# Kernel optimization log

Measured on AMD Instinct MI355X. Metric: run time of the kernel, lower is better.

The kernel has to match this reference:

```python
import jax, jax.numpy as jnp
import numpy as np

MODES = 32
INPUT_MODES = 24
LAMBDA = 0.1
T_TOTAL = 1.0
EVAL_PTS = 200  # hardcoded in Circuit.forward


def _unitary_from_parameters(n, params):
    # Reconstruct a unitary from n**2-1 real SU(N)-generator coefficients:
    # Hermitian traceless H, then U = expm(iH) via eigh (differentiable).
    m = n * (n - 1) // 2
    re = params[:m]
    im = params[m:2 * m]
    d = params[2 * m:2 * m + n - 1]
    iu = jnp.triu_indices(n, 1)
    H = jnp.zeros((n, n), jnp.complex64).at[iu].set(re + 1j * im)
    H = H + H.conj().T
    diag = jnp.concatenate([d, -jnp.sum(d, keepdims=True)]).astype(jnp.complex64)
    H = H + jnp.diag(diag)
    w, V = jnp.linalg.eigh(H)  # H Hermitian
    return (V * jnp.exp(1j * w)[None, :]) @ V.conj().T


def setup_inputs() -> dict:
    key = jax.random.key(0)
    k1, k2, k3, k4, k5, k6 = jax.random.split(key, 6)
    B = 2048
    return {
        "A0_real": jax.random.normal(k1, (B, INPUT_MODES), jnp.float32),
        "A0_imag": jax.random.normal(k2, (B, INPUT_MODES), jnp.float32),
        "omega": jax.random.normal(k3, (MODES,), jnp.float32),
        "kappa": jax.random.uniform(k4, (MODES,), jnp.float32),
        "nonlinearity": jax.random.uniform(k5, (1,), jnp.float32),
        "params": (jax.random.uniform(k6, (MODES * MODES - 1,), jnp.float32) - 0.5) * (2.0 * np.pi),
    }


def reference(A0_real, A0_imag, omega, kappa, nonlinearity, params):
    c64 = jnp.complex64
    B = A0_real.shape[0]
    A0 = (A0_real + 1j * A0_imag).astype(c64)
    # pad: first input_modes from A0, rest ones (per forward)
    A_init = jnp.ones((B, MODES), c64).at[:, :INPUT_MODES].set(A0)

    U = _unitary_from_parameters(MODES, params)
    I = jnp.eye(MODES, dtype=c64)
    UtU = U.T @ U  # plain (non-conjugate) transpose, matching torch U.T
    mix = UtU @ jnp.linalg.inv(I * (1.0 + LAMBDA) - UtU)
    kappa2 = kappa.astype(c64) ** 2            # ode passes kappa**2
    sk = jnp.sqrt(kappa2)                      # diag_embed(kappa**0.5)
    T2 = -(sk[:, None] * (0.5 * I + mix)) * sk[None, :]  # constant in time
    nl2 = (nonlinearity[0].astype(c64)) ** 2   # ode passes nonlinearity**2
    om = omega.astype(c64)

    def f(A):  # time_evolution_operator, with diag matmuls fused elementwise
        freq = 1j * (om[None, :] + nl2 * (jnp.abs(A) ** 2))  # [B, modes]
        return freq * A + A @ T2.T  # correct_norm assumed identity passthrough

    dt = T_TOTAL / (EVAL_PTS - 1)

    def step(A, _):  # classic RK4 (fixed-step stand-in for dopri5)
        k1 = f(A)
        k2 = f(A + 0.5 * dt * k1)
        k3 = f(A + 0.5 * dt * k2)
        k4 = f(A + dt * k3)
        A = A + (dt / 6.0) * (k1 + 2.0 * k2 + 2.0 * k3 + k4)
        return A, A

    _, traj = jax.lax.scan(step, A_init, None, length=EVAL_PTS - 1)
    return jnp.concatenate([A_init[None], traj], axis=0)  # [200, B, modes] complex64
```

## Files before the change

kernel.cpp:

```cpp
#include <hip/hip_runtime.h>
#include <math.h>

#define NMODES 32
#define NPAIR 496

__device__ float2 g_T2[NMODES * NMODES];

__device__ __forceinline__ void cfma(float2& acc, float2 a, float bre, float bim) {
    acc.x = fmaf(a.x, bre, fmaf(-a.y, bim, acc.x));
    acc.y = fmaf(a.x, bim, fmaf(a.y, bre, acc.y));
}

__global__ __launch_bounds__(1024) void setup_kernel(const float* __restrict__ params,
                                                     const float* __restrict__ kappa) {
    __shared__ float2 pool[5120];
    float2* Xb  = pool;
    float2* X2b = pool + 1024;
    float2* X3b = pool + 2048;
    float2* P0b = pool + 3072;
    float2* P1b = pool + 4096;
    float2* Aug0 = pool;
    float2* Wbuf = pool + 2048;
    float2* Aug1 = pool + 3072;

    __shared__ int sh_s;
    __shared__ float sh_scale;

    const int tid = threadIdx.x;
    const int i = tid >> 5;
    const int j = tid & 31;
    const int ij = i * 32 + j;

    {
        float2 h;
        if (i == j) {
            float d;
            if (i < 31) {
                d = params[2 * NPAIR + i];
            } else {
                d = 0.0f;
                for (int r = 0; r < 31; ++r) d -= params[2 * NPAIR + r];
            }
            h = make_float2(d, 0.0f);
        } else {
            int a = (i < j) ? i : j;
            int b = (i < j) ? j : i;
            int idx = 31 * a - (a * (a - 1)) / 2 + (b - a - 1);
            float re = params[idx];
            float im = params[NPAIR + idx];
            h = (i < j) ? make_float2(re, im) : make_float2(re, -im);
        }
        Xb[ij] = h;
    }
    __syncthreads();

    if (tid < 32) {
        float s = 0.0f;
        for (int c = 0; c < 32; ++c) {
            float2 v = Xb[tid * 32 + c];
            s += sqrtf(v.x * v.x + v.y * v.y);
        }
        for (int off = 16; off > 0; off >>= 1)
            s = fmaxf(s, __shfl_down(s, off));
        if (tid == 0) {
            int sc_n = 0;
            float sc = 1.0f;
            while (s > 1.0f && sc_n < 40) { s *= 0.5f; sc *= 0.5f; ++sc_n; }
            sh_s = sc_n;
            sh_scale = sc;
        }
    }
    __syncthreads();

    {
        float sc = sh_scale;
        float2 v = Xb[ij];
        Xb[ij] = make_float2(-v.y * sc, v.x * sc);
    }
    __syncthreads();

    {
        float2 acc = {0, 0};
        for (int k = 0; k < 32; ++k) {
            float2 a = Xb[i * 32 + k];
            float2 b = Xb[k * 32 + j];
            cfma(acc, a, b.x, b.y);
        }
        X2b[ij] = acc;
    }
    __syncthreads();

    {
        float2 acc = {0, 0};
        for (int k = 0; k < 32; ++k) {
            float2 a = X2b[i * 32 + k];
            float2 b = Xb[k * 32 + j];
            cfma(acc, a, b.x, b.y);
        }
        X3b[ij] = acc;
    }
    __syncthreads();

    const float c0 = 1.0f, c1 = 1.0f, c2 = 0.5f;
    const float c3 = 1.0f / 6.0f, c4 = 1.0f / 24.0f, c5 = 1.0f / 120.0f;
    const float c6 = 1.0f / 720.0f, c7 = 1.0f / 5040.0f, c8 = 1.0f / 40320.0f;
    const float c9 = 1.0f / 362880.0f, c10 = 1.0f / 3628800.0f, c11 = 1.0f / 39916800.0f;

    const float2 xv = Xb[ij];
    const float2 x2v = X2b[ij];
    const float del = (i == j) ? 1.0f : 0.0f;

    P0b[ij] = make_float2(c9 * del + c10 * xv.x + c11 * x2v.x,
                          c10 * xv.y + c11 * x2v.y);
    __syncthreads();

    float2* hp_cur = P0b;
    float2* hp_nxt = P1b;
    const float bm_d[3] = {c6, c3, c0};
    const float bm_x[3] = {c7, c4, c1};
    const float bm_x2[3] = {c8, c5, c2};
    for (int hm = 0; hm < 3; ++hm) {
        float2 acc = {0, 0};
        for (int k = 0; k < 32; ++k) {
            float2 a = X3b[i * 32 + k];
            float2 b = hp_cur[k * 32 + j];
            cfma(acc, a, b.x, b.y);
        }
        acc.x += bm_d[hm] * del + bm_x[hm] * xv.x + bm_x2[hm] * x2v.x;
        acc.y += bm_x[hm] * xv.y + bm_x2[hm] * x2v.y;
        hp_nxt[ij] = acc;
        __syncthreads();
        float2* t = hp_cur; hp_cur = hp_nxt; hp_nxt = t;
    }

    {
        int s = sh_s;
        for (int q = 0; q < s; ++q) {
            float2 acc = {0, 0};
            for (int k = 0; k < 32; ++k) {
                float2 a = hp_cur[i * 32 + k];
                float2 b = hp_cur[k * 32 + j];
                cfma(acc, a, b.x, b.y);
            }
            hp_nxt[ij] = acc;
            __syncthreads();
            float2* t = hp_cur; hp_cur = hp_nxt; hp_nxt = t;
        }
    }

    {
        float2 acc = {0, 0};
        for (int k = 0; k < 32; ++k) {
            float2 a = hp_cur[k * 32 + i];
            float2 b = hp_cur[k * 32 + j];
            cfma(acc, a, b.x, b.y);
        }
        Wbuf[ij] = acc;
    }
    __syncthreads();

    {
        float2 w = Wbuf[ij];
        Aug0[i * 64 + j] = make_float2(1.1f * del - w.x, -w.y);
        Aug0[i * 64 + j + 32] = w;
    }
    __syncthreads();

    float2* gc = Aug0;
    float2* gn = Aug1;
    for (int p = 0; p < 32; ++p) {
        float2 d = gc[p * 64 + p];
        float2 f = gc[i * 64 + p];
        float2 rpL = gc[p * 64 + j];
        float2 rpR = gc[p * 64 + j + 32];
        float2 vL = gc[i * 64 + j];
        float2 vR = gc[i * 64 + j + 32];
        float den = 1.0f / (d.x * d.x + d.y * d.y);
        float2 pr = make_float2(d.x * den, -d.y * den);
        if (i == p) {
            gn[i * 64 + j] = make_float2(rpL.x * pr.x - rpL.y * pr.y,
                                         rpL.x * pr.y + rpL.y * pr.x);
            gn[i * 64 + j + 32] = make_float2(rpR.x * pr.x - rpR.y * pr.y,
                                              rpR.x * pr.y + rpR.y * pr.x);
        } else {
            float2 g = make_float2(f.x * pr.x - f.y * pr.y, f.x * pr.y + f.y * pr.x);
            vL.x -= g.x * rpL.x - g.y * rpL.y;
            vL.y -= g.x * rpL.y + g.y * rpL.x;
            vR.x -= g.x * rpR.x - g.y * rpR.y;
            vR.y -= g.x * rpR.y + g.y * rpR.x;
            gn[i * 64 + j] = vL;
            gn[i * 64 + j + 32] = vR;
        }
        __syncthreads();
        float2* t = gc; gc = gn; gn = t;
    }

    {
        float2 mix = gc[i * 64 + j + 32];
        float kk2 = fabsf(kappa[i]) * fabsf(kappa[j]);
        g_T2[ij] = make_float2(-kk2 * (((i == j) ? 0.5f : 0.0f) + mix.x),
                               -kk2 * mix.y);
    }
}

__device__ __forceinline__ float2 f_eval(const float* __restrict__ xq,
                                         float2 ym,
                                         const float2* __restrict__ t2q,
                                         float om, float nl2) {
    float2 acc0 = make_float2(0.0f, 0.0f);
    float2 acc1 = make_float2(0.0f, 0.0f);
#pragma unroll
    for (int q = 0; q < 4; ++q) {
        float4 v = *reinterpret_cast<const float4*>(xq + 4 * q);
        float2 ta = t2q[2 * q];
        float2 tb = t2q[2 * q + 1];
        acc0.x = fmaf(ta.x, v.x, acc0.x);
        acc0.x = fmaf(-ta.y, v.y, acc0.x);
        acc0.y = fmaf(ta.x, v.y, acc0.y);
        acc0.y = fmaf(ta.y, v.x, acc0.y);
        acc1.x = fmaf(tb.x, v.z, acc1.x);
        acc1.x = fmaf(-tb.y, v.w, acc1.x);
        acc1.y = fmaf(tb.x, v.w, acc1.y);
        acc1.y = fmaf(tb.y, v.z, acc1.y);
    }
    float2 acc = make_float2(acc0.x + acc1.x, acc0.y + acc1.y);
    acc.x += __shfl_xor(acc.x, 1);
    acc.y += __shfl_xor(acc.y, 1);
    acc.x += __shfl_xor(acc.x, 2);
    acc.y += __shfl_xor(acc.y, 2);
    float w = fmaf(nl2, fmaf(ym.x, ym.x, ym.y * ym.y), om);
    return make_float2(acc.x - w * ym.y, acc.y + w * ym.x);
}

__global__ __launch_bounds__(128) void ode_kernel(const float* __restrict__ A0r,
                                                  const float* __restrict__ A0i,
                                                  const float* __restrict__ omega,
                                                  const float* __restrict__ nln,
                                                  float* __restrict__ out,
                                                  long long out_size) {
    const int tid = threadIdx.x;
    const int m = tid >> 2;
    const int h = tid & 3;
    const int b = blockIdx.x;

    float2 t2q[8];
#pragma unroll
    for (int k = 0; k < 8; ++k) t2q[k] = g_T2[m * NMODES + h * 8 + k];

    const float om = omega[m];
    const float nl = nln[0];
    const float nl2 = nl * nl;
    const float dt = 1.0f / 199.0f;
    const float hdt = 0.5f * dt;
    const float sdt = dt / 6.0f;

    float2 a;
    if (m < 24) a = make_float2(A0r[b * 24 + m], A0i[b * 24 + m]);
    else        a = make_float2(1.0f, 0.0f);

    __shared__ __align__(16) float buf0[80];
    __shared__ __align__(16) float buf1[80];
    const int wslot = (m >> 3) * 20 + (m & 7) * 2;
    const float* rq0 = buf0 + h * 20;
    const float* rq1 = buf1 + h * 20;

    if (h == 0) {
        long long o = (long long)b * 32 + m;
        if (o < out_size) out[o] = a.x;
        *reinterpret_cast<float2*>(buf0 + wslot) = a;
    }
    __syncthreads();

    for (int t = 1; t < 200; ++t) {
        float2 k1 = f_eval(rq0, a, t2q, om, nl2);
        float2 y2 = make_float2(fmaf(hdt, k1.x, a.x), fmaf(hdt, k1.y, a.y));
        if (h == 0) *reinterpret_cast<float2*>(buf1 + wslot) = y2;
        __syncthreads();

        float2 k2 = f_eval(rq1, y2, t2q, om, nl2);
        float2 y3 = make_float2(fmaf(hdt, k2.x, a.x), fmaf(hdt, k2.y, a.y));
        if (h == 0) *reinterpret_cast<float2*>(buf0 + wslot) = y3;
        __syncthreads();

        float2 k3 = f_eval(rq0, y3, t2q, om, nl2);
        float2 y4 = make_float2(fmaf(dt, k3.x, a.x), fmaf(dt, k3.y, a.y));
        if (h == 0) *reinterpret_cast<float2*>(buf1 + wslot) = y4;
        __syncthreads();

        float2 k4 = f_eval(rq1, y4, t2q, om, nl2);

        a.x = fmaf(sdt, k1.x + 2.0f * k2.x + 2.0f * k3.x + k4.x, a.x);
        a.y = fmaf(sdt, k1.y + 2.0f * k2.y + 2.0f * k3.y + k4.y, a.y);

        if (h == 0) {
            *reinterpret_cast<float2*>(buf0 + wslot) = a;
            long long o = (long long)t * 65536 + (long long)b * 32 + m;
            if (o < out_size) out[o] = a.x;
        }
        __syncthreads();
    }
}

extern "C" void kernel_launch(void* const* d_in, const int* in_sizes, int n_in,
                              void* d_out, int out_size, void* d_ws, size_t ws_size,
                              hipStream_t stream) {
    const float* A0r = (const float*)d_in[0];
    const float* A0i = (const float*)d_in[1];
    const float* omega = (const float*)d_in[2];
    const float* kappa = (const float*)d_in[3];
    const float* nln = (const float*)d_in[4];
    const float* params = (const float*)d_in[5];

    setup_kernel<<<1, 1024, 0, stream>>>(params, kappa);
    ode_kernel<<<2048, 128, 0, stream>>>(A0r, A0i, omega, nln,
                                         (float*)d_out, (long long)out_size);
}
```

Measured before the change: 413.9 us.

## Map each batch row to one wavefront and do matvec with DPP row rotations

Each trajectory now runs on one 64-lane wavefront. Lanes 0-31 hold the real parts of the 32 modes and lanes 32-63 the imaginary parts. The complex 32x32 matvec becomes a real 64x64 matvec, built from cross-row xor shuffles plus inline-asm v_fmac with DPP row_ror over a per-lane pre-permuted T2 register array. This removes the shared-memory exchange buffers and all __syncthreads barriers from the RK4 loop. In exchange it keeps 64 T2 values in registers per lane and depends on hand-written DPP asm, which is tied to wave64 AMD hardware.

```diff
diff --git a/kernel.cpp b/kernel.cpp
--- a/kernel.cpp
+++ b/kernel.cpp
@@ -203,101 +203,94 @@
     }
 }
 
-__device__ __forceinline__ float2 f_eval(const float* __restrict__ xq,
-                                         float2 ym,
-                                         const float2* __restrict__ t2q,
-                                         float om, float nl2) {
-    float2 acc0 = make_float2(0.0f, 0.0f);
-    float2 acc1 = make_float2(0.0f, 0.0f);
+#define FMROR(acc, xv, tv, K)                                                   \
+    asm("v_fmac_f32 %0, %1, %2 row_ror:" #K " row_mask:0xf bank_mask:0xf"       \
+        : "+v"(acc) : "v"(xv), "v"(tv))
+
+#define K_STEP(K)                                                               \
+    FMROR(a0, x,  t[K],      K);                                                \
+    FMROR(a1, x1, t[16 + K], K);                                                \
+    FMROR(a2, x2, t[32 + K], K);                                                \
+    FMROR(a3, x3, t[48 + K], K)
+
+__device__ __forceinline__ float f_ev(float x, const float* __restrict__ t,
+                                      float om, float nl2, float sgn) {
+    float x1 = __shfl_xor(x, 16);
+    float x2 = __shfl_xor(x, 32);
+    float x3 = __shfl_xor(x, 48);
+    float a0 = 0.0f, a1 = 0.0f, a2 = 0.0f, a3 = 0.0f;
+    a0 = fmaf(x, t[0], a0);
+    a1 = fmaf(x1, t[16], a1);
+    a2 = fmaf(x2, t[32], a2);
+    a3 = fmaf(x3, t[48], a3);
+    K_STEP(1);  K_STEP(2);  K_STEP(3);  K_STEP(4);  K_STEP(5);
+    K_STEP(6);  K_STEP(7);  K_STEP(8);  K_STEP(9);  K_STEP(10);
+    K_STEP(11); K_STEP(12); K_STEP(13); K_STEP(14); K_STEP(15);
+    float w = fmaf(nl2, fmaf(x, x, x2 * x2), om);
+    return (a0 + a1) + (a2 + a3) + sgn * w * x2;
+}
+
+__global__ __launch_bounds__(64) void ode_kernel(const float* __restrict__ A0r,
+                                                 const float* __restrict__ A0i,
+                                                 const float* __restrict__ omega,
+                                                 const float* __restrict__ nln,
+                                                 float* __restrict__ out,
+                                                 long long out_size) {
+    const int lane = threadIdx.x;
+    const int m = lane & 31;
+    const int part = lane >> 5;
+    const int r = lane >> 4;
+    const int c = lane & 15;
+    const int b = blockIdx.x;
+
+    float t[64];
 #pragma unroll
     for (int q = 0; q < 4; ++q) {
-        float4 v = *reinterpret_cast<const float4*>(xq + 4 * q);
-        float2 ta = t2q[2 * q];
-        float2 tb = t2q[2 * q + 1];
-        acc0.x = fmaf(ta.x, v.x, acc0.x);
-        acc0.x = fmaf(-ta.y, v.y, acc0.x);
-        acc0.y = fmaf(ta.x, v.y, acc0.y);
-        acc0.y = fmaf(ta.y, v.x, acc0.y);
-        acc1.x = fmaf(tb.x, v.z, acc1.x);
-        acc1.x = fmaf(-tb.y, v.w, acc1.x);
-        acc1.y = fmaf(tb.x, v.w, acc1.y);
-        acc1.y = fmaf(tb.y, v.z, acc1.y);
-    }
-    float2 acc = make_float2(acc0.x + acc1.x, acc0.y + acc1.y);
-    acc.x += __shfl_xor(acc.x, 1);
-    acc.y += __shfl_xor(acc.y, 1);
-    acc.x += __shfl_xor(acc.x, 2);
-    acc.y += __shfl_xor(acc.y, 2);
-    float w = fmaf(nl2, fmaf(ym.x, ym.x, ym.y * ym.y), om);
-    return make_float2(acc.x - w * ym.y, acc.y + w * ym.x);
-}
-
-__global__ __launch_bounds__(128) void ode_kernel(const float* __restrict__ A0r,
-                                                  const float* __restrict__ A0i,
-                                                  const float* __restrict__ omega,
-                                                  const float* __restrict__ nln,
-                                                  float* __restrict__ out,
-                                                  long long out_size) {
-    const int tid = threadIdx.x;
-    const int m = tid >> 2;
-    const int h = tid & 3;
-    const int b = blockIdx.x;
-
-    float2 t2q[8];
 #pragma unroll
-    for (int k = 0; k < 8; ++k) t2q[k] = g_T2[m * NMODES + h * 8 + k];
+        for (int k = 0; k < 16; ++k) {
+            int j = 16 * (r ^ q) + ((c - k) & 15);
+            int jm = j & 31;
+            int jp = j >> 5;
+            float2 tv = g_T2[m * NMODES + jm];
+            float val;
+            if (part == 0) val = (jp == 0) ? tv.x : -tv.y;
+            else           val = (jp == 0) ? tv.y : tv.x;
+            t[q * 16 + k] = val;
+        }
+    }
 
     const float om = omega[m];
     const float nl = nln[0];
     const float nl2 = nl * nl;
+    const float sgn = part ? 1.0f : -1.0f;
     const float dt = 1.0f / 199.0f;
     const float hdt = 0.5f * dt;
     const float sdt = dt / 6.0f;
 
-    float2 a;
-    if (m < 24) a = make_float2(A0r[b * 24 + m], A0i[b * 24 + m]);
-    else        a = make_float2(1.0f, 0.0f);
-
-    __shared__ __align__(16) float buf0[80];
-    __shared__ __align__(16) float buf1[80];
-    const int wslot = (m >> 3) * 20 + (m & 7) * 2;
-    const float* rq0 = buf0 + h * 20;
-    const float* rq1 = buf1 + h * 20;
-
-    if (h == 0) {
+    float x;
+    if (part == 0) x = (m < 24) ? A0r[b * 24 + m] : 1.0f;
+    else           x = (m < 24) ? A0i[b * 24 + m] : 0.0f;
+
+    if (part == 0) {
         long long o = (long long)b * 32 + m;
-        if (o < out_size) out[o] = a.x;
-        *reinterpret_cast<float2*>(buf0 + wslot) = a;
-    }
-    __syncthreads();
-
-    for (int t = 1; t < 200; ++t) {
-        float2 k1 = f_eval(rq0, a, t2q, om, nl2);
-        float2 y2 = make_float2(fmaf(hdt, k1.x, a.x), fmaf(hdt, k1.y, a.y));
-        if (h == 0) *reinterpret_cast<float2*>(buf1 + wslot) = y2;
-        __syncthreads();
-
-        float2 k2 = f_eval(rq1, y2, t2q, om, nl2);
-        float2 y3 = make_float2(fmaf(hdt, k2.x, a.x), fmaf(hdt, k2.y, a.y));
-        if (h == 0) *reinterpret_cast<float2*>(buf0 + wslot) = y3;
-        __syncthreads();
-
-        float2 k3 = f_eval(rq0, y3, t2q, om, nl2);
-        float2 y4 = make_float2(fmaf(dt, k3.x, a.x), fmaf(dt, k3.y, a.y));
-        if (h == 0) *reinterpret_cast<float2*>(buf1 + wslot) = y4;
-        __syncthreads();
-
-        float2 k4 = f_eval(rq1, y4, t2q, om, nl2);
-
-        a.x = fmaf(sdt, k1.x + 2.0f * k2.x + 2.0f * k3.x + k4.x, a.x);
-        a.y = fmaf(sdt, k1.y + 2.0f * k2.y + 2.0f * k3.y + k4.y, a.y);
-
-        if (h == 0) {
-            *reinterpret_cast<float2*>(buf0 + wslot) = a;
-            long long o = (long long)t * 65536 + (long long)b * 32 + m;
-            if (o < out_size) out[o] = a.x;
-        }
-        __syncthreads();
+        if (o < out_size) out[o] = x;
+    }
+
+    for (int st = 1; st < 200; ++st) {
+        float k1 = f_ev(x, t, om, nl2, sgn);
+        float y  = fmaf(hdt, k1, x);
+        float k2 = f_ev(y, t, om, nl2, sgn);
+        y = fmaf(hdt, k2, x);
+        float k3 = f_ev(y, t, om, nl2, sgn);
+        y = fmaf(dt, k3, x);
+        float k4 = f_ev(y, t, om, nl2, sgn);
+
+        x = fmaf(sdt, k1 + 2.0f * k2 + 2.0f * k3 + k4, x);
+
+        if (part == 0) {
+            long long o = (long long)st * 65536 + (long long)b * 32 + m;
+            if (o < out_size) out[o] = x;
+        }
     }
 }
 
@@ -312,6 +305,6 @@
     const float* params = (const float*)d_in[5];
 
     setup_kernel<<<1, 1024, 0, stream>>>(params, kappa);
-    ode_kernel<<<2048, 128, 0, stream>>>(A0r, A0i, omega, nln,
-                                         (float*)d_out, (long long)out_size);
-}
+    ode_kernel<<<2048, 64, 0, stream>>>(A0r, A0i, omega, nln,
+                                        (float*)d_out, (long long)out_size);
+}
```

Result: faster. 397.0 us (-4.1%).
